# Performance work log

Measured on AMD Instinct MI355X. Metric: run time of the kernel, lower is better.

Reference implementation:

```python
import jax, jax.numpy as jnp
import numpy as np

BN_EPS = 1e-5

def _sage_conv(x, src, dst, Wl, bl, Wr):
    # mean aggregation of neighbor messages: agg[v] = mean_{u->v} x[u]
    n = x.shape[0]
    s = jax.ops.segment_sum(x[src], dst, num_segments=n)            # [N, d]
    cnt = jax.ops.segment_sum(jnp.ones_like(dst, dtype=x.dtype), dst, num_segments=n)
    agg = s / jnp.maximum(cnt, 1.0)[:, None]
    return agg @ Wl + bl + x @ Wr                                   # lin_l(agg) + lin_r(x)

def _bn(x, g, b):
    mu = jnp.mean(x, axis=0)
    var = jnp.var(x, axis=0)
    return (x - mu) * jax.lax.rsqrt(var + BN_EPS) * g + b

def setup_inputs() -> dict:
    key = jax.random.key(0)
    ks = jax.random.split(key, 8)
    N, E, D, H, C = 100000, 1600000, 128, 128, 47
    sc = 1.0 / np.sqrt(D)
    return {
        "x": jax.random.normal(ks[0], (N, D), jnp.float32),
        "edge_index": jax.random.randint(ks[1], (2, E), 0, N, jnp.int64),
        "Wl0": jax.random.normal(ks[2], (D, H), jnp.float32) * sc,
        "bl0": jnp.zeros((H,), jnp.float32),
        "Wr0": jax.random.normal(ks[3], (D, H), jnp.float32) * sc,
        "g0": jnp.ones((H,), jnp.float32),
        "be0": jnp.zeros((H,), jnp.float32),
        "Wl1": jax.random.normal(ks[4], (H, H), jnp.float32) * sc,
        "bl1": jnp.zeros((H,), jnp.float32),
        "Wr1": jax.random.normal(ks[5], (H, H), jnp.float32) * sc,
        "g1": jnp.ones((H,), jnp.float32),
        "be1": jnp.zeros((H,), jnp.float32),
        "Wl2": jax.random.normal(ks[6], (H, C), jnp.float32) * sc,
        "bl2": jnp.zeros((C,), jnp.float32),
        "Wr2": jax.random.normal(ks[7], (H, C), jnp.float32) * sc,
    }

def reference(x, edge_index, Wl0, bl0, Wr0, g0, be0, Wl1, bl1, Wr1, g1, be1, Wl2, bl2, Wr2):
    src, dst = edge_index[0], edge_index[1]
    h = _sage_conv(x, src, dst, Wl0, bl0, Wr0)
    h = jax.nn.relu(_bn(h, g0, be0))
    h = _sage_conv(h, src, dst, Wl1, bl1, Wr1)
    h = jax.nn.relu(_bn(h, g1, be1))
    h = _sage_conv(h, src, dst, Wl2, bl2, Wr2)
    return jax.nn.log_softmax(h, axis=-1)
```

## Files before the change

### kernel.cpp

```cpp
#include <hip/hip_runtime.h>
#include <hip/hip_fp8.h>
#include <stdint.h>

#define AS1 __attribute__((address_space(1)))
#define AS3 __attribute__((address_space(3)))

typedef __bf16 bf16;
typedef __bf16 bf16x2 __attribute__((ext_vector_type(2)));
typedef __bf16 bf16x4v __attribute__((ext_vector_type(4)));
typedef __bf16 bf16x8 __attribute__((ext_vector_type(8)));
typedef float f32x4 __attribute__((ext_vector_type(4)));
typedef float f32x2 __attribute__((ext_vector_type(2)));
typedef __hip_fp8_e4m3 fp8;

#define BN_EPS 1e-5f
#define BKT_SHIFT 8
#define BKT_NODES 256
#define TILE_E 2048
#define NCOPY 16

__global__ void k_setup(const float* __restrict__ x, bf16* __restrict__ x_bf,
                        unsigned char* __restrict__ x8, int n4,
                        const int* __restrict__ ei, int* __restrict__ btot, int E, int nbkt,
                        const float* __restrict__ Wl0, const float* __restrict__ Wr0,
                        const float* __restrict__ Wl1, const float* __restrict__ Wr1,
                        const float* __restrict__ Wl2, const float* __restrict__ Wr2,
                        bf16* __restrict__ Bt0, bf16* __restrict__ Bt1, bf16* __restrict__ Bt2) {
    __shared__ int hist[512];
    const int tid = threadIdx.x;
    int g = blockIdx.x * 256 + tid;
    if (g < n4) {
        float4 v = ((const float4*)x)[g];
        bf16x4v o; o[0] = (bf16)v.x; o[1] = (bf16)v.y; o[2] = (bf16)v.z; o[3] = (bf16)v.w;
        ((bf16x4v*)x_bf)[g] = o;
        uchar4 o8;
        o8.x = fp8(v.x).__x; o8.y = fp8(v.y).__x; o8.z = fp8(v.z).__x; o8.w = fp8(v.w).__x;
        ((uchar4*)x8)[g] = o8;
    }
    if (blockIdx.x < 128) {
        int idx = g;
        int c = idx >> 8, k = idx & 255;
        float v0 = (k < 128) ? Wl0[k * 128 + c] : Wr0[(k - 128) * 128 + c];
        Bt0[c * 256 + k] = (bf16)v0;
        float v1 = (k < 128) ? Wl1[k * 128 + c] : Wr1[(k - 128) * 128 + c];
        Bt1[c * 256 + k] = (bf16)v1;
        if (k < 128) {
            float v2 = 0.f;
            if (c < 47)      v2 = Wl2[k * 47 + c];
            else if (c < 94) v2 = Wr2[k * 47 + (c - 47)];
            Bt2[c * 128 + k] = (bf16)v2;
        }
    }
    int nbinb = (E + 4095) / 4096;
    if (blockIdx.x < nbinb) {
        hist[tid] = 0; hist[tid + 256] = 0;
        __syncthreads();
        const int e0 = blockIdx.x * 4096;
        #pragma unroll
        for (int k = 0; k < 4; ++k) {
            int i4 = (e0 >> 2) + k * 256 + tid;
            if (i4 * 4 + 3 < E) {
                int4 d4 = ((const int4*)(ei + E))[i4];
                atomicAdd(&hist[d4.x >> BKT_SHIFT], 1);
                atomicAdd(&hist[d4.y >> BKT_SHIFT], 1);
                atomicAdd(&hist[d4.z >> BKT_SHIFT], 1);
                atomicAdd(&hist[d4.w >> BKT_SHIFT], 1);
            } else {
                for (int e = i4 * 4; e < min(E, i4 * 4 + 4); ++e)
                    atomicAdd(&hist[ei[E + e] >> BKT_SHIFT], 1);
            }
        }
        __syncthreads();
        for (int b = tid; b < nbkt; b += 256)
            if (hist[b]) atomicAdd(&btot[b], hist[b]);
    }
}

__device__ __forceinline__ void scan_btot(const int* __restrict__ btot, int nbkt,
                                          int* sb, int* wsum) {
    const int tid = threadIdx.x, lane = tid & 63, wid = tid >> 6;
    int a = (tid < nbkt) ? btot[tid] : 0;
    int b2 = (tid + 256 < nbkt) ? btot[tid + 256] : 0;
    int ia = a, ib = b2;
    #pragma unroll
    for (int d = 1; d < 64; d <<= 1) {
        int t1 = __shfl_up(ia, d, 64);
        int t2 = __shfl_up(ib, d, 64);
        if (lane >= d) { ia += t1; ib += t2; }
    }
    if (lane == 63) { wsum[wid] = ia; wsum[4 + wid] = ib; }
    __syncthreads();
    if (tid == 0) {
        int c = 0;
        #pragma unroll
        for (int i = 0; i < 8; ++i) { int t = wsum[i]; wsum[i] = c; c += t; }
    }
    __syncthreads();
    sb[tid] = ia - a + wsum[wid];
    sb[tid + 256] = ib - b2 + wsum[4 + wid];
    if (tid == 255) sb[512] = ib + wsum[7];
    __syncthreads();
}

__global__ __launch_bounds__(256) void k_bin(const int* __restrict__ ei,
                                             const int* __restrict__ btot,
                                             int* __restrict__ bfill,
                                             uint32_t* __restrict__ pair_buf,
                                             int E, int nbkt) {
    __shared__ int hist[512], gbase[512], hcur[512];
    __shared__ int sb[513], wsum[8];
    const int tid = threadIdx.x;
    const int e0 = blockIdx.x * TILE_E;
    hist[tid] = 0; hist[tid + 256] = 0;
    scan_btot(btot, nbkt, sb, wsum);

    int dreg[TILE_E / 256];
    #pragma unroll
    for (int k = 0; k < TILE_E / 256; ++k) {
        int e = e0 + k * 256 + tid;
        int d = (e < E) ? ei[E + e] : -1;
        dreg[k] = d;
        if (d >= 0) atomicAdd(&hist[d >> BKT_SHIFT], 1);
    }
    __syncthreads();

    for (int b = tid; b < nbkt; b += 256) {
        int h = hist[b];
        int g = (h > 0) ? atomicAdd(&bfill[b], h) : 0;
        gbase[b] = sb[b] + g;
        hcur[b] = 0;
    }
    __syncthreads();

    #pragma unroll
    for (int k = 0; k < TILE_E / 256; ++k) {
        int d = dreg[k];
        if (d >= 0) {
            int e = e0 + k * 256 + tid;
            int s = ei[e];
            int b = d >> BKT_SHIFT;
            int r = atomicAdd(&hcur[b], 1);
            pair_buf[(size_t)gbase[b] + r] =
                ((uint32_t)s << BKT_SHIFT) | (uint32_t)(d & (BKT_NODES - 1));
        }
    }
}

__global__ __launch_bounds__(256) void k_fill2(const uint32_t* __restrict__ pair_buf,
                                               const int* __restrict__ btot,
                                               int* __restrict__ row_ptr,
                                               float* __restrict__ inv_deg,
                                               int* __restrict__ col_idx,
                                               int n, int E, int nbkt) {
    __shared__ int hist[256], excl[256], hcur[256], wsum4[4];
    __shared__ int sb[513], wsum[8];
    const int b = blockIdx.x;
    const int tid = threadIdx.x, lane = tid & 63, wid = tid >> 6;
    const int n0 = b << BKT_SHIFT;
    hist[tid] = 0; hcur[tid] = 0;
    scan_btot(btot, nbkt, sb, wsum);
    const int s = sb[b], e = sb[b + 1];
    for (int i = s + tid; i < e; i += 256)
        atomicAdd(&hist[pair_buf[i] & (BKT_NODES - 1)], 1);
    __syncthreads();
    int v = hist[tid];
    int incl = v;
    #pragma unroll
    for (int d = 1; d < 64; d <<= 1) {
        int t = __shfl_up(incl, d, 64);
        if (lane >= d) incl += t;
    }
    if (lane == 63) wsum4[wid] = incl;
    __syncthreads();
    if (tid == 0) {
        int c = 0;
        #pragma unroll
        for (int i = 0; i < 4; ++i) { int t = wsum4[i]; wsum4[i] = c; c += t; }
    }
    __syncthreads();
    int ex = incl - v + wsum4[wid];
    excl[tid] = ex;
    int node = n0 + tid;
    if (node < n) {
        row_ptr[node] = s + ex;
        inv_deg[node] = 1.0f / (float)(v > 1 ? v : 1);
    }
    if (b == (int)gridDim.x - 1 && tid == 0) row_ptr[n] = E;
    __syncthreads();
    for (int i = s + tid; i < e; i += 256) {
        uint32_t pk = pair_buf[i];
        int dl = pk & (BKT_NODES - 1);
        int r = atomicAdd(&hcur[dl], 1);
        col_idx[s + excl[dl] + r] = (int)(pk >> BKT_SHIFT);
    }
}

__global__ void k_aggregate(const unsigned char* __restrict__ src8, bf16* __restrict__ dst,
                            const int* __restrict__ row_ptr, const int* __restrict__ col_idx,
                            const float* __restrict__ inv_deg, int n) {
    int node = blockIdx.x * 4 + (threadIdx.x >> 6);
    int lane = threadIdx.x & 63;
    if (node >= n) return;
    int e0 = row_ptr[node], e1 = row_ptr[node + 1];
    float inv = inv_deg[node];
    const uint32_t l2 = (uint32_t)(lane << 1);
    float f0 = 0.f, f1 = 0.f;
    int e = e0;
    for (; e < e1 && (e & 3); ++e) {
        uint32_t u = *(const uint16_t*)(src8 + (((uint32_t)col_idx[e] << 7) + l2));
        f32x2 p = __builtin_amdgcn_cvt_pk_f32_fp8(u, false);
        f0 += p[0]; f1 += p[1];
    }
    for (; e + 7 < e1; e += 8) {
        int4 i0 = *(const int4*)(col_idx + e);
        int4 i1 = *(const int4*)(col_idx + e + 4);
        uint32_t u0 = *(const uint16_t*)(src8 + (((uint32_t)i0.x << 7) + l2));
        uint32_t u1 = *(const uint16_t*)(src8 + (((uint32_t)i0.y << 7) + l2));
        uint32_t u2 = *(const uint16_t*)(src8 + (((uint32_t)i0.z << 7) + l2));
        uint32_t u3 = *(const uint16_t*)(src8 + (((uint32_t)i0.w << 7) + l2));
        uint32_t u4 = *(const uint16_t*)(src8 + (((uint32_t)i1.x << 7) + l2));
        uint32_t u5 = *(const uint16_t*)(src8 + (((uint32_t)i1.y << 7) + l2));
        uint32_t u6 = *(const uint16_t*)(src8 + (((uint32_t)i1.z << 7) + l2));
        uint32_t u7 = *(const uint16_t*)(src8 + (((uint32_t)i1.w << 7) + l2));
        f32x2 p0 = __builtin_amdgcn_cvt_pk_f32_fp8(u0, false);
        f32x2 p1 = __builtin_amdgcn_cvt_pk_f32_fp8(u1, false);
        f32x2 p2 = __builtin_amdgcn_cvt_pk_f32_fp8(u2, false);
        f32x2 p3 = __builtin_amdgcn_cvt_pk_f32_fp8(u3, false);
        f32x2 p4 = __builtin_amdgcn_cvt_pk_f32_fp8(u4, false);
        f32x2 p5 = __builtin_amdgcn_cvt_pk_f32_fp8(u5, false);
        f32x2 p6 = __builtin_amdgcn_cvt_pk_f32_fp8(u6, false);
        f32x2 p7 = __builtin_amdgcn_cvt_pk_f32_fp8(u7, false);
        f0 += ((p0[0] + p1[0]) + (p2[0] + p3[0])) + ((p4[0] + p5[0]) + (p6[0] + p7[0]));
        f1 += ((p0[1] + p1[1]) + (p2[1] + p3[1])) + ((p4[1] + p5[1]) + (p6[1] + p7[1]));
    }
    if (e + 3 < e1) {
        int4 i0 = *(const int4*)(col_idx + e);
        uint32_t u0 = *(const uint16_t*)(src8 + (((uint32_t)i0.x << 7) + l2));
        uint32_t u1 = *(const uint16_t*)(src8 + (((uint32_t)i0.y << 7) + l2));
        uint32_t u2 = *(const uint16_t*)(src8 + (((uint32_t)i0.z << 7) + l2));
        uint32_t u3 = *(const uint16_t*)(src8 + (((uint32_t)i0.w << 7) + l2));
        f32x2 p0 = __builtin_amdgcn_cvt_pk_f32_fp8(u0, false);
        f32x2 p1 = __builtin_amdgcn_cvt_pk_f32_fp8(u1, false);
        f32x2 p2 = __builtin_amdgcn_cvt_pk_f32_fp8(u2, false);
        f32x2 p3 = __builtin_amdgcn_cvt_pk_f32_fp8(u3, false);
        f0 += (p0[0] + p1[0]) + (p2[0] + p3[0]);
        f1 += (p0[1] + p1[1]) + (p2[1] + p3[1]);
        e += 4;
    }
    for (; e < e1; ++e) {
        uint32_t u = *(const uint16_t*)(src8 + (((uint32_t)col_idx[e] << 7) + l2));
        f32x2 p = __builtin_amdgcn_cvt_pk_f32_fp8(u, false);
        f0 += p[0]; f1 += p[1];
    }
    bf16x2 o; o[0] = (bf16)(f0 * inv); o[1] = (bf16)(f1 * inv);
    *(bf16x2*)(dst + (size_t)node * 128 + (lane << 1)) = o;
}

template<int CH, bool STATS, int NT>
__global__ __launch_bounds__(256) void k_gemm6(
    const bf16* __restrict__ A1, const bf16* __restrict__ A2, const bf16* __restrict__ Bt,
    const float* __restrict__ bias, bf16* __restrict__ outH,
    fp8* __restrict__ yl8, bf16* __restrict__ yrbf, float* __restrict__ stats, int M) {
    __shared__ __attribute__((aligned(16))) bf16 sA[2][4096];
    __shared__ __attribute__((aligned(16))) bf16 sB[2][4096];
    __shared__ float scol[128], scol2[128];
    constexpr int LDB = CH * 32;
    const int tid = threadIdx.x;
    const int w = tid >> 6, l = tid & 63;
    const int q = l >> 4, r = l & 15;
    const int r0 = blockIdx.x * 128;
    if (STATS && tid < 128) { scol[tid] = 0.f; scol2[tid] = 0.f; }

    auto stage = [&](int buf, int c) {
        const bf16* As = (c < 4) ? A1 : A2;
        const int ka = (c & 3) * 32;
        #pragma unroll
        for (int i = 0; i < 2; ++i) {
            const int T = w * 2 + i;
            const bf16* ga = As + (size_t)(r0 + T * 16 + r) * 128 + ka + q * 8;
            __builtin_amdgcn_global_load_lds((AS1 uint32_t*)(uintptr_t)ga,
                (AS3 uint32_t*)(uint32_t)(uintptr_t)(&sA[buf][T * 512]), 16, 0, 0);
            if (T < NT) {
                const bf16* gb = Bt + (T * 16 + r) * LDB + c * 32 + q * 8;
                __builtin_amdgcn_global_load_lds((AS1 uint32_t*)(uintptr_t)gb,
                    (AS3 uint32_t*)(uint32_t)(uintptr_t)(&sB[buf][T * 512]), 16, 0, 0);
            }
        }
    };

    f32x4 acc[2][NT];
    #pragma unroll
    for (int i = 0; i < 2; ++i)
        #pragma unroll
        for (int j = 0; j < NT; ++j) { acc[i][j][0] = 0.f; acc[i][j][1] = 0.f; acc[i][j][2] = 0.f; acc[i][j][3] = 0.f; }

    stage(0, 0);
    __syncthreads();

    #pragma unroll
    for (int c = 0; c < CH; ++c) {
        const int cur = c & 1;
        if (c + 1 < CH) stage(cur ^ 1, c + 1);
        bf16x8 af0 = *(const bf16x8*)&sA[cur][(w * 2 + 0) * 512 + q * 128 + r * 8];
        bf16x8 af1 = *(const bf16x8*)&sA[cur][(w * 2 + 1) * 512 + q * 128 + r * 8];
        #pragma unroll
        for (int ct = 0; ct < NT; ++ct) {
            bf16x8 bv = *(const bf16x8*)&sB[cur][ct * 512 + q * 128 + r * 8];
            acc[0][ct] = __builtin_amdgcn_mfma_f32_16x16x32_bf16(af0, bv, acc[0][ct], 0, 0, 0);
            acc[1][ct] = __builtin_amdgcn_mfma_f32_16x16x32_bf16(af1, bv, acc[1][ct], 0, 0, 0);
        }
        __syncthreads();
    }

    if (STATS) {
        #pragma unroll
        for (int ct = 0; ct < NT; ++ct) {
            int col = ct * 16 + r;
            float bv = bias ? bias[col] : 0.f;
            float s_c = 0.f, q_c = 0.f;
            #pragma unroll
            for (int rt = 0; rt < 2; ++rt) {
                #pragma unroll
                for (int j = 0; j < 4; ++j) {
                    int row = r0 + w * 32 + rt * 16 + q * 4 + j;
                    if (row < M) {
                        float v = acc[rt][ct][j] + bv;
                        outH[(size_t)row * 128 + col] = (bf16)v;
                        s_c += v; q_c += v * v;
                    }
                }
            }
            atomicAdd(&scol[col], s_c);
            atomicAdd(&scol2[col], q_c);
        }
        __syncthreads();
        float* sbase = stats + ((blockIdx.x & (NCOPY - 1)) << 8);
        if (tid < 128) {
            atomicAdd(&sbase[tid], scol[tid]);
            atomicAdd(&sbase[128 + tid], scol2[tid]);
        }
    } else {
        #pragma unroll
        for (int rt = 0; rt < 2; ++rt) {
            #pragma unroll
            for (int ct = 0; ct < NT; ++ct) {
                int col = ct * 16 + r;
                #pragma unroll
                for (int j = 0; j < 4; ++j) {
                    int row = r0 + w * 32 + rt * 16 + q * 4 + j;
                    if (row >= M) continue;
                    if (col < 47)      yl8[(size_t)row * 64 + col] = fp8(acc[rt][ct][j]);
                    else if (col < 94) yrbf[(size_t)row * 48 + (col - 47)] = (bf16)acc[rt][ct][j];
                }
            }
        }
    }
}

__global__ void k_bn_prep(const float* __restrict__ sums, const float* __restrict__ gma,
                          const float* __restrict__ bta, float* __restrict__ scsh, int n) {
    int col = threadIdx.x;
    float s = 0.f, q = 0.f;
    #pragma unroll
    for (int cpy = 0; cpy < NCOPY; ++cpy) {
        s += sums[(cpy << 8) + col];
        q += sums[(cpy << 8) + 128 + col];
    }
    float invn = 1.0f / (float)n;
    float mu = s * invn;
    float var = q * invn - mu * mu;
    float sc = gma[col] * rsqrtf(var + BN_EPS);
    scsh[col] = sc;
    scsh[128 + col] = bta[col] - mu * sc;
}

__global__ void k_bn_apply(const bf16* __restrict__ h, const float* __restrict__ scsh,
                           bf16* __restrict__ out, unsigned char* __restrict__ out8, int n) {
    int g = blockIdx.x * blockDim.x + threadIdx.x;
    int row = g >> 6, c2 = g & 63;
    if (row >= n) return;
    int col = c2 << 1;
    float2 sc = *(const float2*)(scsh + col);
    float2 sh = *(const float2*)(scsh + 128 + col);
    bf16x2 hv = *(const bf16x2*)(h + (size_t)row * 128 + col);
    float r0 = fmaxf((float)hv[0] * sc.x + sh.x, 0.f);
    float r1 = fmaxf((float)hv[1] * sc.y + sh.y, 0.f);
    bf16x2 o; o[0] = (bf16)r0; o[1] = (bf16)r1;
    *(bf16x2*)(out + (size_t)row * 128 + col) = o;
    uchar2 o8; o8.x = fp8(r0).__x; o8.y = fp8(r1).__x;
    *(uchar2*)(out8 + (size_t)row * 128 + col) = o8;
}

__global__ void k_final(const unsigned char* __restrict__ yl, const bf16* __restrict__ yr,
                        const int* __restrict__ row_ptr, const int* __restrict__ col_idx,
                        const float* __restrict__ inv_deg, const float* __restrict__ bl2,
                        float* __restrict__ out, int n) {
    int node = blockIdx.x * 4 + (threadIdx.x >> 6);
    int lane = threadIdx.x & 63;
    if (node >= n) return;
    int e0 = row_ptr[node], e1 = row_ptr[node + 1];
    float inv = inv_deg[node];
    const int sub = lane >> 4;
    const int c4 = lane & 15;
    const uint32_t loff = (uint32_t)(c4 << 2);
    float a0 = 0.f, a1 = 0.f, a2 = 0.f, a3 = 0.f;
    int base = e0;
    for (; base + 16 <= e1; base += 16) {
        int i0 = col_idx[base + sub];
        int i1 = col_idx[base + 4 + sub];
        int i2 = col_idx[base + 8 + sub];
        int i3 = col_idx[base + 12 + sub];
        uint32_t u0 = *(const uint32_t*)(yl + (((uint32_t)i0 << 6) + loff));
        uint32_t u1 = *(const uint32_t*)(yl + (((uint32_t)i1 << 6) + loff));
        uint32_t u2 = *(const uint32_t*)(yl + (((uint32_t)i2 << 6) + loff));
        uint32_t u3 = *(const uint32_t*)(yl + (((uint32_t)i3 << 6) + loff));
        f32x2 p0l = __builtin_amdgcn_cvt_pk_f32_fp8(u0, false);
        f32x2 p0h = __builtin_amdgcn_cvt_pk_f32_fp8(u0, true);
        f32x2 p1l = __builtin_amdgcn_cvt_pk_f32_fp8(u1, false);
        f32x2 p1h = __builtin_amdgcn_cvt_pk_f32_fp8(u1, true);
        f32x2 p2l = __builtin_amdgcn_cvt_pk_f32_fp8(u2, false);
        f32x2 p2h = __builtin_amdgcn_cvt_pk_f32_fp8(u2, true);
        f32x2 p3l = __builtin_amdgcn_cvt_pk_f32_fp8(u3, false);
        f32x2 p3h = __builtin_amdgcn_cvt_pk_f32_fp8(u3, true);
        a0 += (p0l[0] + p1l[0]) + (p2l[0] + p3l[0]);
        a1 += (p0l[1] + p1l[1]) + (p2l[1] + p3l[1]);
        a2 += (p0h[0] + p1h[0]) + (p2h[0] + p3h[0]);
        a3 += (p0h[1] + p1h[1]) + (p2h[1] + p3h[1]);
    }
    if (base < e1) {
        int ee0 = base + sub;
        int ee1 = base + 4 + sub;
        int ee2 = base + 8 + sub;
        int ee3 = base + 12 + sub;
        bool k0 = ee0 < e1, k1 = ee1 < e1, k2 = ee2 < e1, k3 = ee3 < e1;
        int i0 = col_idx[k0 ? ee0 : e0];
        int i1 = col_idx[k1 ? ee1 : e0];
        int i2 = col_idx[k2 ? ee2 : e0];
        int i3 = col_idx[k3 ? ee3 : e0];
        uint32_t u0 = *(const uint32_t*)(yl + (((uint32_t)i0 << 6) + loff));
        uint32_t u1 = *(const uint32_t*)(yl + (((uint32_t)i1 << 6) + loff));
        uint32_t u2 = *(const uint32_t*)(yl + (((uint32_t)i2 << 6) + loff));
        uint32_t u3 = *(const uint32_t*)(yl + (((uint32_t)i3 << 6) + loff));
        u0 = k0 ? u0 : 0u;
        u1 = k1 ? u1 : 0u;
        u2 = k2 ? u2 : 0u;
        u3 = k3 ? u3 : 0u;
        f32x2 p0l = __builtin_amdgcn_cvt_pk_f32_fp8(u0, false);
        f32x2 p0h = __builtin_amdgcn_cvt_pk_f32_fp8(u0, true);
        f32x2 p1l = __builtin_amdgcn_cvt_pk_f32_fp8(u1, false);
        f32x2 p1h = __builtin_amdgcn_cvt_pk_f32_fp8(u1, true);
        f32x2 p2l = __builtin_amdgcn_cvt_pk_f32_fp8(u2, false);
        f32x2 p2h = __builtin_amdgcn_cvt_pk_f32_fp8(u2, true);
        f32x2 p3l = __builtin_amdgcn_cvt_pk_f32_fp8(u3, false);
        f32x2 p3h = __builtin_amdgcn_cvt_pk_f32_fp8(u3, true);
        a0 += (p0l[0] + p1l[0]) + (p2l[0] + p3l[0]);
        a1 += (p0l[1] + p1l[1]) + (p2l[1] + p3l[1]);
        a2 += (p0h[0] + p1h[0]) + (p2h[0] + p3h[0]);
        a3 += (p0h[1] + p1h[1]) + (p2h[1] + p3h[1]);
    }
    a0 += __shfl_xor(a0, 16, 64); a1 += __shfl_xor(a1, 16, 64);
    a2 += __shfl_xor(a2, 16, 64); a3 += __shfl_xor(a3, 16, 64);
    a0 += __shfl_xor(a0, 32, 64); a1 += __shfl_xor(a1, 32, 64);
    a2 += __shfl_xor(a2, 32, 64); a3 += __shfl_xor(a3, 32, 64);
    const int f0 = c4 << 2;
    bf16x4v yv4 = *(const bf16x4v*)(yr + (size_t)node * 48 + f0);
    float v0 = (f0 + 0 < 47) ? fmaf(a0, inv, (float)yv4[0] + bl2[f0 + 0]) : -__builtin_inff();
    float v1 = (f0 + 1 < 47) ? fmaf(a1, inv, (float)yv4[1] + bl2[f0 + 1]) : -__builtin_inff();
    float v2 = (f0 + 2 < 47) ? fmaf(a2, inv, (float)yv4[2] + bl2[f0 + 2]) : -__builtin_inff();
    float v3 = (f0 + 3 < 47) ? fmaf(a3, inv, (float)yv4[3] + bl2[f0 + 3]) : -__builtin_inff();
    float m = fmaxf(fmaxf(v0, v1), fmaxf(v2, v3));
    #pragma unroll
    for (int o = 1; o < 16; o <<= 1) m = fmaxf(m, __shfl_xor(m, o, 64));
    float ex0 = (f0 + 0 < 47) ? __expf(v0 - m) : 0.f;
    float ex1 = (f0 + 1 < 47) ? __expf(v1 - m) : 0.f;
    float ex2 = (f0 + 2 < 47) ? __expf(v2 - m) : 0.f;
    float ex3 = (f0 + 3 < 47) ? __expf(v3 - m) : 0.f;
    float s = (ex0 + ex1) + (ex2 + ex3);
    #pragma unroll
    for (int o = 1; o < 16; o <<= 1) s += __shfl_xor(s, o, 64);
    float ls = __logf(s);
    if (lane < 16) {
        float* op = out + (size_t)node * 47 + f0;
        if (f0 + 0 < 47) op[0] = v0 - m - ls;
        if (f0 + 1 < 47) op[1] = v1 - m - ls;
        if (f0 + 2 < 47) op[2] = v2 - m - ls;
        if (f0 + 3 < 47) op[3] = v3 - m - ls;
    }
}

extern "C" void kernel_launch(void* const* d_in, const int* in_sizes, int n_in,
                              void* d_out, int out_size, void* d_ws, size_t ws_size,
                              hipStream_t stream) {
    const float* x   = (const float*)d_in[0];
    const int*   ei  = (const int*)d_in[1];
    const float* Wl0 = (const float*)d_in[2];
    const float* bl0 = (const float*)d_in[3];
    const float* Wr0 = (const float*)d_in[4];
    const float* g0  = (const float*)d_in[5];
    const float* be0 = (const float*)d_in[6];
    const float* Wl1 = (const float*)d_in[7];
    const float* bl1 = (const float*)d_in[8];
    const float* Wr1 = (const float*)d_in[9];
    const float* g1  = (const float*)d_in[10];
    const float* be1 = (const float*)d_in[11];
    const float* Wl2 = (const float*)d_in[12];
    const float* bl2 = (const float*)d_in[13];
    const float* Wr2 = (const float*)d_in[14];
    float* out = (float*)d_out;

    const int N  = in_sizes[0] / 128;
    const int E  = in_sizes[1] / 2;
    const int NP = ((N + 127) / 128) * 128;
    const int NBKT = (N + BKT_NODES - 1) / BKT_NODES;

    char* p = (char*)d_ws;
    size_t off = 0;
    auto alloc = [&](size_t b) { char* r = p + off; off += (b + 255) & ~(size_t)255; return r; };
    int*   bfill   = (int*)alloc(1024 * 4);
    float* bnsum   = (float*)alloc(2 * NCOPY * 256 * 4);
    int*   btot    = (int*)alloc(512 * 4);
    size_t zero_span = off;
    float* scsh    = (float*)alloc(2 * 256 * 4);
    int*   row_ptr = (int*)alloc((size_t)(N + 1) * 4);
    float* invd    = (float*)alloc((size_t)N * 4);
    int*   col_idx = (int*)alloc((size_t)E * 4);
    uint32_t* pair_buf = (uint32_t*)alloc((size_t)E * 4);
    bf16*  x_bf    = (bf16*)alloc((size_t)NP * 128 * 2);
    bf16*  aggbf   = (bf16*)alloc((size_t)NP * 128 * 2);
    bf16*  hbf     = (bf16*)alloc((size_t)NP * 128 * 2);
    unsigned char* h8 = (unsigned char*)alloc((size_t)NP * 128);
    float* bufF    = (float*)alloc((size_t)NP * 128 * 4 + 256);
    bf16*  Bt0     = (bf16*)alloc(128 * 256 * 2);
    bf16*  Bt1     = (bf16*)alloc(128 * 256 * 2);
    bf16*  Bt2     = (bf16*)alloc(128 * 128 * 2);
    unsigned char* x8 = (unsigned char*)bufF;
    bf16*  hraw = (bf16*)bufF;
    fp8*   yl8  = (fp8*)bufF;
    bf16*  yrbf = (bf16*)((char*)bufF + (size_t)NP * 64);

    hipMemsetAsync(bfill, 0, zero_span, stream);

    int n4 = N * 128 / 4;
    k_setup<<<(n4 + 255) / 256, 256, 0, stream>>>(x, x_bf, x8, n4, ei, btot, E, NBKT,
                                                  Wl0, Wr0, Wl1, Wr1, Wl2, Wr2, Bt0, Bt1, Bt2);
    k_bin<<<(E + TILE_E - 1) / TILE_E, 256, 0, stream>>>(ei, btot, bfill, pair_buf, E, NBKT);
    k_fill2<<<NBKT, 256, 0, stream>>>(pair_buf, btot, row_ptr, invd, col_idx, N, E, NBKT);

    int aggBlocks  = (N + 3) / 4;
    int gemmBlocks = NP / 128;
    int bnBlocks   = (N * 64 + 255) / 256;

    k_aggregate<<<aggBlocks, 256, 0, stream>>>(x8, aggbf, row_ptr, col_idx, invd, N);
    k_gemm6<8, true, 8><<<gemmBlocks, 256, 0, stream>>>(aggbf, x_bf, Bt0, bl0, hraw, nullptr, nullptr, bnsum, N);
    k_bn_prep<<<1, 128, 0, stream>>>(bnsum, g0, be0, scsh, N);
    k_bn_apply<<<bnBlocks, 256, 0, stream>>>(hraw, scsh, hbf, h8, N);
    k_aggregate<<<aggBlocks, 256, 0, stream>>>(h8, aggbf, row_ptr, col_idx, invd, N);
    k_gemm6<8, true, 8><<<gemmBlocks, 256, 0, stream>>>(aggbf, hbf, Bt1, bl1, hraw, nullptr, nullptr, bnsum + NCOPY * 256, N);
    k_bn_prep<<<1, 128, 0, stream>>>(bnsum + NCOPY * 256, g1, be1, scsh + 256, N);
    k_bn_apply<<<bnBlocks, 256, 0, stream>>>(hraw, scsh + 256, hbf, h8, N);
    k_gemm6<4, false, 6><<<gemmBlocks, 256, 0, stream>>>(hbf, hbf, Bt2, nullptr, nullptr, yl8, yrbf, nullptr, N);
    k_final<<<aggBlocks, 256, 0, stream>>>((const unsigned char*)yl8, yrbf, row_ptr, col_idx, invd, bl2, out, N);
}
```

Measured before the change: 492.9 us.

## Process two nodes per wavefront in aggregation with 4-byte gathers and masked tail

```diff
diff --git a/kernel.cpp b/kernel.cpp
--- a/kernel.cpp
+++ b/kernel.cpp
@@ -195,66 +195,96 @@
     }
 }
 
+#define ACC4(u) { f32x2 pl_ = __builtin_amdgcn_cvt_pk_f32_fp8(u, false); \
+                  f32x2 ph_ = __builtin_amdgcn_cvt_pk_f32_fp8(u, true);  \
+                  a0 += pl_[0]; a1 += pl_[1]; a2 += ph_[0]; a3 += ph_[1]; }
 __global__ void k_aggregate(const unsigned char* __restrict__ src8, bf16* __restrict__ dst,
                             const int* __restrict__ row_ptr, const int* __restrict__ col_idx,
                             const float* __restrict__ inv_deg, int n) {
-    int node = blockIdx.x * 4 + (threadIdx.x >> 6);
-    int lane = threadIdx.x & 63;
-    if (node >= n) return;
-    int e0 = row_ptr[node], e1 = row_ptr[node + 1];
-    float inv = inv_deg[node];
-    const uint32_t l2 = (uint32_t)(lane << 1);
-    float f0 = 0.f, f1 = 0.f;
-    int e = e0;
-    for (; e < e1 && (e & 3); ++e) {
-        uint32_t u = *(const uint16_t*)(src8 + (((uint32_t)col_idx[e] << 7) + l2));
-        f32x2 p = __builtin_amdgcn_cvt_pk_f32_fp8(u, false);
-        f0 += p[0]; f1 += p[1];
-    }
-    for (; e + 7 < e1; e += 8) {
+    const int lane = threadIdx.x & 63;
+    const int half = lane >> 5;
+    const int sl = lane & 31;
+    const int node = blockIdx.x * 8 + ((threadIdx.x >> 6) << 1) + half;
+    const bool valid = node < n;
+    const int nn = valid ? node : 0;
+    const int re0 = row_ptr[nn];
+    const int re1 = valid ? row_ptr[nn + 1] : re0;
+    const float inv = inv_deg[nn];
+    const uint32_t l4 = (uint32_t)(sl << 2);
+    float a0 = 0.f, a1 = 0.f, a2 = 0.f, a3 = 0.f;
+    int e = re0;
+    for (; e < re1 && (e & 3); ++e) {
+        uint32_t u = *(const uint32_t*)(src8 + (((uint32_t)col_idx[e] << 7) + l4));
+        ACC4(u)
+    }
+    for (; e + 16 <= re1; e += 16) {
         int4 i0 = *(const int4*)(col_idx + e);
         int4 i1 = *(const int4*)(col_idx + e + 4);
-        uint32_t u0 = *(const uint16_t*)(src8 + (((uint32_t)i0.x << 7) + l2));
-        uint32_t u1 = *(const uint16_t*)(src8 + (((uint32_t)i0.y << 7) + l2));
-        uint32_t u2 = *(const uint16_t*)(src8 + (((uint32_t)i0.z << 7) + l2));
-        uint32_t u3 = *(const uint16_t*)(src8 + (((uint32_t)i0.w << 7) + l2));
-        uint32_t u4 = *(const uint16_t*)(src8 + (((uint32_t)i1.x << 7) + l2));
-        uint32_t u5 = *(const uint16_t*)(src8 + (((uint32_t)i1.y << 7) + l2));
-        uint32_t u6 = *(const uint16_t*)(src8 + (((uint32_t)i1.z << 7) + l2));
-        uint32_t u7 = *(const uint16_t*)(src8 + (((uint32_t)i1.w << 7) + l2));
-        f32x2 p0 = __builtin_amdgcn_cvt_pk_f32_fp8(u0, false);
-        f32x2 p1 = __builtin_amdgcn_cvt_pk_f32_fp8(u1, false);
-        f32x2 p2 = __builtin_amdgcn_cvt_pk_f32_fp8(u2, false);
-        f32x2 p3 = __builtin_amdgcn_cvt_pk_f32_fp8(u3, false);
-        f32x2 p4 = __builtin_amdgcn_cvt_pk_f32_fp8(u4, false);
-        f32x2 p5 = __builtin_amdgcn_cvt_pk_f32_fp8(u5, false);
-        f32x2 p6 = __builtin_amdgcn_cvt_pk_f32_fp8(u6, false);
-        f32x2 p7 = __builtin_amdgcn_cvt_pk_f32_fp8(u7, false);
-        f0 += ((p0[0] + p1[0]) + (p2[0] + p3[0])) + ((p4[0] + p5[0]) + (p6[0] + p7[0]));
-        f1 += ((p0[1] + p1[1]) + (p2[1] + p3[1])) + ((p4[1] + p5[1]) + (p6[1] + p7[1]));
-    }
-    if (e + 3 < e1) {
+        int4 i2 = *(const int4*)(col_idx + e + 8);
+        int4 i3 = *(const int4*)(col_idx + e + 12);
+        uint32_t u0  = *(const uint32_t*)(src8 + (((uint32_t)i0.x << 7) + l4));
+        uint32_t u1  = *(const uint32_t*)(src8 + (((uint32_t)i0.y << 7) + l4));
+        uint32_t u2  = *(const uint32_t*)(src8 + (((uint32_t)i0.z << 7) + l4));
+        uint32_t u3  = *(const uint32_t*)(src8 + (((uint32_t)i0.w << 7) + l4));
+        uint32_t u4  = *(const uint32_t*)(src8 + (((uint32_t)i1.x << 7) + l4));
+        uint32_t u5  = *(const uint32_t*)(src8 + (((uint32_t)i1.y << 7) + l4));
+        uint32_t u6  = *(const uint32_t*)(src8 + (((uint32_t)i1.z << 7) + l4));
+        uint32_t u7  = *(const uint32_t*)(src8 + (((uint32_t)i1.w << 7) + l4));
+        uint32_t u8  = *(const uint32_t*)(src8 + (((uint32_t)i2.x << 7) + l4));
+        uint32_t u9  = *(const uint32_t*)(src8 + (((uint32_t)i2.y << 7) + l4));
+        uint32_t u10 = *(const uint32_t*)(src8 + (((uint32_t)i2.z << 7) + l4));
+        uint32_t u11 = *(const uint32_t*)(src8 + (((uint32_t)i2.w << 7) + l4));
+        uint32_t u12 = *(const uint32_t*)(src8 + (((uint32_t)i3.x << 7) + l4));
+        uint32_t u13 = *(const uint32_t*)(src8 + (((uint32_t)i3.y << 7) + l4));
+        uint32_t u14 = *(const uint32_t*)(src8 + (((uint32_t)i3.z << 7) + l4));
+        uint32_t u15 = *(const uint32_t*)(src8 + (((uint32_t)i3.w << 7) + l4));
+        ACC4(u0) ACC4(u1) ACC4(u2) ACC4(u3) ACC4(u4) ACC4(u5) ACC4(u6) ACC4(u7)
+        ACC4(u8) ACC4(u9) ACC4(u10) ACC4(u11) ACC4(u12) ACC4(u13) ACC4(u14) ACC4(u15)
+    }
+    if (e < re1) {
         int4 i0 = *(const int4*)(col_idx + e);
-        uint32_t u0 = *(const uint16_t*)(src8 + (((uint32_t)i0.x << 7) + l2));
-        uint32_t u1 = *(const uint16_t*)(src8 + (((uint32_t)i0.y << 7) + l2));
-        uint32_t u2 = *(const uint16_t*)(src8 + (((uint32_t)i0.z << 7) + l2));
-        uint32_t u3 = *(const uint16_t*)(src8 + (((uint32_t)i0.w << 7) + l2));
-        f32x2 p0 = __builtin_amdgcn_cvt_pk_f32_fp8(u0, false);
-        f32x2 p1 = __builtin_amdgcn_cvt_pk_f32_fp8(u1, false);
-        f32x2 p2 = __builtin_amdgcn_cvt_pk_f32_fp8(u2, false);
-        f32x2 p3 = __builtin_amdgcn_cvt_pk_f32_fp8(u3, false);
-        f0 += (p0[0] + p1[0]) + (p2[0] + p3[0]);
-        f1 += (p0[1] + p1[1]) + (p2[1] + p3[1]);
-        e += 4;
-    }
-    for (; e < e1; ++e) {
-        uint32_t u = *(const uint16_t*)(src8 + (((uint32_t)col_idx[e] << 7) + l2));
-        f32x2 p = __builtin_amdgcn_cvt_pk_f32_fp8(u, false);
-        f0 += p[0]; f1 += p[1];
-    }
-    bf16x2 o; o[0] = (bf16)(f0 * inv); o[1] = (bf16)(f1 * inv);
-    *(bf16x2*)(dst + (size_t)node * 128 + (lane << 1)) = o;
-}
+        int4 i1 = *(const int4*)(col_idx + e + 4);
+        int4 i2 = *(const int4*)(col_idx + e + 8);
+        int4 i3 = *(const int4*)(col_idx + e + 12);
+        bool k0  = e + 0  < re1, k1  = e + 1  < re1, k2  = e + 2  < re1, k3  = e + 3  < re1;
+        bool k4  = e + 4  < re1, k5  = e + 5  < re1, k6  = e + 6  < re1, k7  = e + 7  < re1;
+        bool k8  = e + 8  < re1, k9  = e + 9  < re1, k10 = e + 10 < re1, k11 = e + 11 < re1;
+        bool k12 = e + 12 < re1, k13 = e + 13 < re1, k14 = e + 14 < re1, k15 = e + 15 < re1;
+        int r0  = k0  ? i0.x : 0, r1  = k1  ? i0.y : 0, r2  = k2  ? i0.z : 0, r3  = k3  ? i0.w : 0;
+        int r4  = k4  ? i1.x : 0, r5  = k5  ? i1.y : 0, r6  = k6  ? i1.z : 0, r7  = k7  ? i1.w : 0;
+        int r8  = k8  ? i2.x : 0, r9  = k9  ? i2.y : 0, r10 = k10 ? i2.z : 0, r11 = k11 ? i2.w : 0;
+        int r12 = k12 ? i3.x : 0, r13 = k13 ? i3.y : 0, r14 = k14 ? i3.z : 0, r15 = k15 ? i3.w : 0;
+        uint32_t u0  = *(const uint32_t*)(src8 + (((uint32_t)r0  << 7) + l4));
+        uint32_t u1  = *(const uint32_t*)(src8 + (((uint32_t)r1  << 7) + l4));
+        uint32_t u2  = *(const uint32_t*)(src8 + (((uint32_t)r2  << 7) + l4));
+        uint32_t u3  = *(const uint32_t*)(src8 + (((uint32_t)r3  << 7) + l4));
+        uint32_t u4  = *(const uint32_t*)(src8 + (((uint32_t)r4  << 7) + l4));
+        uint32_t u5  = *(const uint32_t*)(src8 + (((uint32_t)r5  << 7) + l4));
+        uint32_t u6  = *(const uint32_t*)(src8 + (((uint32_t)r6  << 7) + l4));
+        uint32_t u7  = *(const uint32_t*)(src8 + (((uint32_t)r7  << 7) + l4));
+        uint32_t u8  = *(const uint32_t*)(src8 + (((uint32_t)r8  << 7) + l4));
+        uint32_t u9  = *(const uint32_t*)(src8 + (((uint32_t)r9  << 7) + l4));
+        uint32_t u10 = *(const uint32_t*)(src8 + (((uint32_t)r10 << 7) + l4));
+        uint32_t u11 = *(const uint32_t*)(src8 + (((uint32_t)r11 << 7) + l4));
+        uint32_t u12 = *(const uint32_t*)(src8 + (((uint32_t)r12 << 7) + l4));
+        uint32_t u13 = *(const uint32_t*)(src8 + (((uint32_t)r13 << 7) + l4));
+        uint32_t u14 = *(const uint32_t*)(src8 + (((uint32_t)r14 << 7) + l4));
+        uint32_t u15 = *(const uint32_t*)(src8 + (((uint32_t)r15 << 7) + l4));
+        u0  = k0  ? u0  : 0u; u1  = k1  ? u1  : 0u; u2  = k2  ? u2  : 0u; u3  = k3  ? u3  : 0u;
+        u4  = k4  ? u4  : 0u; u5  = k5  ? u5  : 0u; u6  = k6  ? u6  : 0u; u7  = k7  ? u7  : 0u;
+        u8  = k8  ? u8  : 0u; u9  = k9  ? u9  : 0u; u10 = k10 ? u10 : 0u; u11 = k11 ? u11 : 0u;
+        u12 = k12 ? u12 : 0u; u13 = k13 ? u13 : 0u; u14 = k14 ? u14 : 0u; u15 = k15 ? u15 : 0u;
+        ACC4(u0) ACC4(u1) ACC4(u2) ACC4(u3) ACC4(u4) ACC4(u5) ACC4(u6) ACC4(u7)
+        ACC4(u8) ACC4(u9) ACC4(u10) ACC4(u11) ACC4(u12) ACC4(u13) ACC4(u14) ACC4(u15)
+    }
+    if (valid) {
+        bf16x4v o;
+        o[0] = (bf16)(a0 * inv); o[1] = (bf16)(a1 * inv);
+        o[2] = (bf16)(a2 * inv); o[3] = (bf16)(a3 * inv);
+        *(bf16x4v*)(dst + (size_t)node * 128 + (sl << 2)) = o;
+    }
+}
+#undef ACC4
 
 template<int CH, bool STATS, int NT>
 __global__ __launch_bounds__(256) void k_gemm6(
@@ -546,9 +576,10 @@
     k_bin<<<(E + TILE_E - 1) / TILE_E, 256, 0, stream>>>(ei, btot, bfill, pair_buf, E, NBKT);
     k_fill2<<<NBKT, 256, 0, stream>>>(pair_buf, btot, row_ptr, invd, col_idx, N, E, NBKT);
 
-    int aggBlocks  = (N + 3) / 4;
+    int aggBlocks  = (N + 7) / 8;
     int gemmBlocks = NP / 128;
     int bnBlocks   = (N * 64 + 255) / 256;
+    int finBlocks  = (N + 3) / 4;
 
     k_aggregate<<<aggBlocks, 256, 0, stream>>>(x8, aggbf, row_ptr, col_idx, invd, N);
     k_gemm6<8, true, 8><<<gemmBlocks, 256, 0, stream>>>(aggbf, x_bf, Bt0, bl0, hraw, nullptr, nullptr, bnsum, N);
@@ -559,5 +590,5 @@
     k_bn_prep<<<1, 128, 0, stream>>>(bnsum + NCOPY * 256, g1, be1, scsh + 256, N);
     k_bn_apply<<<bnBlocks, 256, 0, stream>>>(hraw, scsh + 256, hbf, h8, N);
     k_gemm6<4, false, 6><<<gemmBlocks, 256, 0, stream>>>(hbf, hbf, Bt2, nullptr, nullptr, yl8, yrbf, nullptr, N);
-    k_final<<<aggBlocks, 256, 0, stream>>>((const unsigned char*)yl8, yrbf, row_ptr, col_idx, invd, bl2, out, N);
-}
+    k_final<<<finBlocks, 256, 0, stream>>>((const unsigned char*)yl8, yrbf, row_ptr, col_idx, invd, bl2, out, N);
+}
```

Measured after the change: 453.3 us. -8.0%, faster.
